# Kernel optimization log

Measured on AMD Instinct MI355X. Metric: run time of the kernel, lower is better.

Reference implementation:

```python
import jax, jax.numpy as jnp
import numpy as np

N_NODES = 50000
N_EDGES = 800000
D_IN, D_HID, D_OUT = 64, 128, 64


def _sage_conv(x, src, dst, W_l, b_l, W_r):
    # PyG SAGEConv (aggr='mean'): out = lin_l(mean_j x_j) + lin_r(x_i)
    msg = x[src]                                    # [E, d] gather
    summed = jax.ops.segment_sum(msg, dst, num_segments=N_NODES)
    cnt = jax.ops.segment_sum(jnp.ones((msg.shape[0], 1), x.dtype), dst,
                              num_segments=N_NODES)
    mean = summed / jnp.maximum(cnt, 1.0)           # [N, d]
    return mean @ W_l + b_l + x @ W_r


def setup_inputs() -> dict:
    key = jax.random.key(0)
    ks = jax.random.split(key, 8)
    x = jax.random.normal(ks[0], (N_NODES, D_IN), dtype=jnp.float32)
    edge_index = jax.random.randint(ks[1], (2, N_EDGES), 0, N_NODES, dtype=jnp.int64)
    s1 = 1.0 / np.sqrt(D_IN)
    s2 = 1.0 / np.sqrt(D_HID)
    W_l1 = jax.random.uniform(ks[2], (D_IN, D_HID), jnp.float32, -s1, s1)
    b_l1 = jnp.zeros((D_HID,), jnp.float32)
    W_r1 = jax.random.uniform(ks[3], (D_IN, D_HID), jnp.float32, -s1, s1)
    W_l2 = jax.random.uniform(ks[4], (D_HID, D_OUT), jnp.float32, -s2, s2)
    b_l2 = jnp.zeros((D_OUT,), jnp.float32)
    W_r2 = jax.random.uniform(ks[5], (D_HID, D_OUT), jnp.float32, -s2, s2)
    return {"x": x, "edge_index": edge_index,
            "W_l1": W_l1, "b_l1": b_l1, "W_r1": W_r1,
            "W_l2": W_l2, "b_l2": b_l2, "W_r2": W_r2}


def reference(x, edge_index, W_l1, b_l1, W_r1, W_l2, b_l2, W_r2):
    src, dst = edge_index[0], edge_index[1]
    h = _sage_conv(x, src, dst, W_l1, b_l1, W_r1)
    h = jax.nn.relu(h)
    # dropout is identity in eval mode (F.dropout(training=self.training))
    out = _sage_conv(h, src, dst, W_l2, b_l2, W_r2)
    return out
```

## Files before the change

kernel.cpp:

```cpp
#include <hip/hip_runtime.h>

namespace {

constexpr int NNODES = 50000;
constexpr int NEDGES = 800000;
constexpr int NBUCK  = (NNODES + 127) / 128;
constexpr int BCAP   = 3072;
constexpr int SB     = 64;
constexpr int CHUNK  = NEDGES / SB;


static __device__ __forceinline__ unsigned short f2bf(float f) {
  unsigned u = __float_as_uint(f);
  u += 0x7FFFu + ((u >> 16) & 1u);
  return (unsigned short)(u >> 16);
}

static __device__ __forceinline__ void pk_fma_lo(float2& d, const float2 a, const float2 b) {
  asm("v_pk_fma_f32 %0, %1, %2, %0 op_sel:[0,0,0] op_sel_hi:[0,1,1]"
      : "+v"(d) : "v"(a), "v"(b));
}
static __device__ __forceinline__ void pk_fma_hi(float2& d, const float2 a, const float2 b) {
  asm("v_pk_fma_f32 %0, %1, %2, %0 op_sel:[1,0,0] op_sel_hi:[1,1,1]"
      : "+v"(d) : "v"(a), "v"(b));
}

static __device__ __forceinline__ int detect_is64_block(const void* raw, int* s_tmp) {
  if (threadIdx.x == 0) *s_tmp = 0;
  __syncthreads();
  const unsigned int* w = (const unsigned int*)raw;
  const int nz = (w[1 + 2 * (int)threadIdx.x] != 0u) ? 1 : 0;
  if (nz) atomicOr(s_tmp, 1);
  __syncthreads();
  return (*s_tmp == 0) ? 1 : 0;
}

__global__ __launch_bounds__(256) void x_to_bf16(const float* __restrict__ xin,
                                                 unsigned short* __restrict__ xb) {
  const int total4 = NNODES * 64 / 4;
  const int stride = gridDim.x * blockDim.x;
  for (int t = blockIdx.x * blockDim.x + threadIdx.x; t < total4; t += stride) {
    const float4 v = ((const float4*)xin)[t];
    ushort4 o;
    o.x = f2bf(v.x); o.y = f2bf(v.y); o.z = f2bf(v.z); o.w = f2bf(v.w);
    ((ushort4*)xb)[t] = o;
  }
}

__global__ __launch_bounds__(512) void hist_pass(const void* __restrict__ raw,
                                                 int* __restrict__ blkhist) {
  __shared__ int hist[NBUCK];
  __shared__ int s_tmp;
  const int is64 = detect_is64_block(raw, &s_tmp);
  for (int i = threadIdx.x; i < NBUCK; i += 512) hist[i] = 0;
  __syncthreads();
  const int b = blockIdx.x;
  const int beg = b * CHUNK, end = beg + CHUNK;
  for (int e = beg + (int)threadIdx.x; e < end; e += 512) {
    const int d = is64 ? (int)((const long long*)raw)[NEDGES + e]
                       : ((const int*)raw)[NEDGES + e];
    atomicAdd(&hist[d >> 7], 1);
  }
  __syncthreads();
  for (int i = threadIdx.x; i < NBUCK; i += 512) blkhist[i * SB + b] = hist[i];
}

__global__ __launch_bounds__(64) void col_scan(const int* __restrict__ blkhist,
                                               int* __restrict__ offs,
                                               int* __restrict__ bcount) {
  const int bk = blockIdx.x;
  const int t = threadIdx.x;
  const int c = blkhist[bk * SB + t];
  int s = c;
#pragma unroll
  for (int off = 1; off < 64; off <<= 1) {
    const int u = __shfl_up(s, off, 64);
    if (t >= off) s += u;
  }
  offs[bk * SB + t] = bk * BCAP + (s - c);
  if (t == 63) bcount[bk] = s;
}

__global__ __launch_bounds__(512) void bucket_prefix(const int* __restrict__ bcount,
                                                     int* __restrict__ bprefix) {
  __shared__ int sh[512];
  const int t = threadIdx.x;
  const int v = (t < NBUCK) ? bcount[t] : 0;
  sh[t] = v;
  __syncthreads();
#pragma unroll
  for (int off = 1; off < 512; off <<= 1) {
    const int val = sh[t];
    const int add = (t >= off) ? sh[t - off] : 0;
    __syncthreads();
    sh[t] = val + add;
    __syncthreads();
  }
  if (t < NBUCK) bprefix[t] = sh[t] - v;
}

__global__ __launch_bounds__(512) void scatter_pass(const void* __restrict__ raw,
                                                    const int* __restrict__ offs,
                                                    unsigned int* __restrict__ ebuf) {
  __shared__ int loff[NBUCK];
  __shared__ int lcur[NBUCK];
  __shared__ int s_tmp;
  const int is64 = detect_is64_block(raw, &s_tmp);
  const int b = blockIdx.x;
  for (int i = threadIdx.x; i < NBUCK; i += 512) {
    loff[i] = offs[i * SB + b];
    lcur[i] = 0;
  }
  __syncthreads();
  const int beg = b * CHUNK, end = beg + CHUNK;
  for (int e = beg + (int)threadIdx.x; e < end; e += 512) {
    int s, d;
    if (is64) {
      const long long* p = (const long long*)raw;
      s = (int)p[e];
      d = (int)p[NEDGES + e];
    } else {
      const int* p = (const int*)raw;
      s = p[e];
      d = p[NEDGES + e];
    }
    const int bk = d >> 7;
    const unsigned int val = ((unsigned int)d << 16) | (unsigned int)s;
    const int lr = atomicAdd(&lcur[bk], 1);
    ebuf[loff[bk] + lr] = val;
  }
}

__global__ __launch_bounds__(256) void csr_emit2(const unsigned int* __restrict__ ebuf,
                                                 const int* __restrict__ bcount,
                                                 const int* __restrict__ bprefix,
                                                 int* __restrict__ row_ptr,
                                                 int* __restrict__ col) {
  const int bk = blockIdx.x;
  const int base = bk * 128;
  const int nloc = min(128, NNODES - base);
  const int cnt = bcount[bk];
  const int bbase = bprefix[bk];
  const unsigned int* eb = ebuf + (size_t)bk * BCAP;

  __shared__ int dcnt[128];
  __shared__ int loff[128];
  __shared__ int lcur[128];
  if (threadIdx.x < 128) dcnt[threadIdx.x] = 0;
  __syncthreads();

  unsigned int vals[12];
  int m = 0;
#pragma unroll
  for (int k = 0; k < 12; ++k) {
    const int e = (int)threadIdx.x + k * 256;
    if (e < cnt) {
      vals[k] = eb[e];
      atomicAdd(&dcnt[(vals[k] >> 16) & 127u], 1);
      m = k + 1;
    }
  }
  __syncthreads();

  if (threadIdx.x < 128) loff[threadIdx.x] = dcnt[threadIdx.x];
  __syncthreads();
#pragma unroll
  for (int off = 1; off < 128; off <<= 1) {
    int add = 0;
    if (threadIdx.x < 128 && (int)threadIdx.x >= off) add = loff[threadIdx.x - off];
    __syncthreads();
    if (threadIdx.x < 128) loff[threadIdx.x] += add;
    __syncthreads();
  }
  if (threadIdx.x < 128) {
    const int excl = loff[threadIdx.x] - dcnt[threadIdx.x];
    loff[threadIdx.x] = excl;
    lcur[threadIdx.x] = 0;
    if ((int)threadIdx.x < nloc) row_ptr[base + threadIdx.x] = bbase + excl;
  }
  if (bk == NBUCK - 1 && threadIdx.x == 0) row_ptr[NNODES] = NEDGES;
  __syncthreads();

#pragma unroll
  for (int k = 0; k < 12; ++k) {
    if (k < m) {
      const int loc = (int)((vals[k] >> 16) & 127u);
      const int slot = bbase + loff[loc] + atomicAdd(&lcur[loc], 1);
      col[slot] = (int)(vals[k] & 0xFFFFu);
    }
  }
}

template <bool FINAL>
__global__ __launch_bounds__(256) void seg_mean_bf(const unsigned int* __restrict__ xb2,
                                                   const int* __restrict__ row_ptr,
                                                   const int* __restrict__ col,
                                                   const float* __restrict__ radd,
                                                   float* __restrict__ outbuf) {
  const int lane = (int)(threadIdx.x & 63);
  const int half = lane >> 5;
  const int c = lane & 31;
  const int wid = (blockIdx.x * blockDim.x + threadIdx.x) >> 6;
  const int nw = (gridDim.x * blockDim.x) >> 6;
  for (int v = wid; v < NNODES; v += nw) {
    const int b = row_ptr[v];
    const int e = row_ptr[v + 1];
    float accx = 0.0f, accy = 0.0f;
    int i = b;
    for (; i + 8 <= e; i += 8) {
      const int s0 = col[i + 0 + half];
      const int s1 = col[i + 2 + half];
      const int s2 = col[i + 4 + half];
      const int s3 = col[i + 6 + half];
      const unsigned int w0 = xb2[(size_t)s0 * 32 + c];
      const unsigned int w1 = xb2[(size_t)s1 * 32 + c];
      const unsigned int w2 = xb2[(size_t)s2 * 32 + c];
      const unsigned int w3 = xb2[(size_t)s3 * 32 + c];
      accx += __uint_as_float(w0 << 16) + __uint_as_float(w1 << 16)
            + __uint_as_float(w2 << 16) + __uint_as_float(w3 << 16);
      accy += __uint_as_float(w0 & 0xFFFF0000u) + __uint_as_float(w1 & 0xFFFF0000u)
            + __uint_as_float(w2 & 0xFFFF0000u) + __uint_as_float(w3 & 0xFFFF0000u);
    }
    for (; i + 2 <= e; i += 2) {
      const unsigned int w0 = xb2[(size_t)col[i + half] * 32 + c];
      accx += __uint_as_float(w0 << 16);
      accy += __uint_as_float(w0 & 0xFFFF0000u);
    }
    if (i < e && half == 0) {
      const unsigned int w0 = xb2[(size_t)col[i] * 32 + c];
      accx += __uint_as_float(w0 << 16);
      accy += __uint_as_float(w0 & 0xFFFF0000u);
    }
    accx += __shfl_xor(accx, 32, 64);
    accy += __shfl_xor(accy, 32, 64);
    if (half == 0) {
      const float inv = 1.0f / fmaxf((float)(e - b), 1.0f);
      float2 res = make_float2(accx * inv, accy * inv);
      const size_t gi = (size_t)v * 32 + c;
      if (FINAL) {
        const float2 ra = ((const float2*)radd)[gi];
        res.x += ra.x; res.y += ra.y;
      }
      ((float2*)outbuf)[gi] = res;
    }
  }
}

template <int MODE>
__global__ __launch_bounds__(256, 3) void gemm128(const float* __restrict__ A0,
                                                  const float* __restrict__ A1,
                                                  const float* __restrict__ W0,
                                                  const float* __restrict__ W1,
                                                  const float* __restrict__ bias,
                                                  float* __restrict__ O0,
                                                  float* __restrict__ O1,
                                                  unsigned short* __restrict__ PB) {
  constexpr int SAS = 36;
  __shared__ float sA[64][SAS];
  __shared__ float sW[32][128];
  const int row0 = blockIdx.x * 64;
  const int tid = threadIdx.x;
  const int r0 = (tid >> 4) * 4;
  const int j0 = (tid & 15) * 4;

  float2 accA2[4][2];
  float2 accB2[4][2];
#pragma unroll
  for (int r = 0; r < 4; ++r)
#pragma unroll
    for (int p = 0; p < 2; ++p) {
      accA2[r][p] = make_float2(0.f, 0.f);
      accB2[r][p] = make_float2(0.f, 0.f);
    }

#pragma unroll 1
  for (int ck = 0; ck < 4; ++ck) {
#pragma unroll
    for (int v = 0; v < 2; ++v) {
      const int vid = v * 256 + tid;
      const int rr = vid >> 3;
      const int kq = (vid & 7) * 4;
      const int grow = row0 + rr;
      float4 val = make_float4(0.f, 0.f, 0.f, 0.f);
      if (grow < NNODES) {
        if (MODE == 0) {
          const float* src = (ck < 2) ? A0 : A1;
          const int kk = (ck & 1) * 32 + kq;
          val = *(const float4*)&src[(size_t)grow * 64 + kk];
        } else {
          val = *(const float4*)&A0[(size_t)grow * 128 + ck * 32 + kq];
        }
      }
      *(float4*)&sA[rr][kq] = val;
    }
#pragma unroll
    for (int v = 0; v < 4; ++v) {
      const int vid = v * 256 + tid;
      const int kk = vid >> 5;
      const int jq = (vid & 31) * 4;
      float4 w;
      if (MODE == 0) {
        const float* src = (ck < 2) ? W0 : W1;
        const int krel = (ck & 1) * 32 + kk;
        w = *(const float4*)&src[(size_t)krel * 128 + jq];
      } else {
        const int kg = ck * 32 + kk;
        const float* src = (jq < 64) ? W0 : W1;
        const int jrel = (jq < 64) ? jq : jq - 64;
        w = *(const float4*)&src[(size_t)kg * 64 + jrel];
      }
      *(float4*)&sW[kk][jq] = w;
    }
    __syncthreads();
#pragma unroll
    for (int k4 = 0; k4 < 8; ++k4) {
      float4 a[4];
#pragma unroll
      for (int r = 0; r < 4; ++r) a[r] = *(const float4*)&sA[r0 + r][k4 * 4];
#pragma unroll
      for (int kp = 0; kp < 2; ++kp) {
        const int k_even = k4 * 4 + kp * 2;
        const float4 wlo0 = *(const float4*)&sW[k_even][j0];
        const float4 whi0 = *(const float4*)&sW[k_even][64 + j0];
        const float4 wlo1 = *(const float4*)&sW[k_even + 1][j0];
        const float4 whi1 = *(const float4*)&sW[k_even + 1][64 + j0];
#pragma unroll
        for (int r = 0; r < 4; ++r) {
          const float2 ap = (kp == 0) ? make_float2(a[r].x, a[r].y)
                                      : make_float2(a[r].z, a[r].w);
          pk_fma_lo(accA2[r][0], ap, make_float2(wlo0.x, wlo0.y));
          pk_fma_lo(accA2[r][1], ap, make_float2(wlo0.z, wlo0.w));
          pk_fma_lo(accB2[r][0], ap, make_float2(whi0.x, whi0.y));
          pk_fma_lo(accB2[r][1], ap, make_float2(whi0.z, whi0.w));
          pk_fma_hi(accA2[r][0], ap, make_float2(wlo1.x, wlo1.y));
          pk_fma_hi(accA2[r][1], ap, make_float2(wlo1.z, wlo1.w));
          pk_fma_hi(accB2[r][0], ap, make_float2(whi1.x, whi1.y));
          pk_fma_hi(accB2[r][1], ap, make_float2(whi1.z, whi1.w));
        }
      }
    }
    __syncthreads();
  }

  float4 blo = make_float4(0.f, 0.f, 0.f, 0.f);
  float4 bhi;
  if (MODE == 0) {
    blo = *(const float4*)&bias[j0];
    bhi = *(const float4*)&bias[64 + j0];
  } else {
    bhi = *(const float4*)&bias[j0];
  }
#pragma unroll
  for (int r = 0; r < 4; ++r) {
    const int grow = row0 + r0 + r;
    if (grow >= NNODES) continue;
    float4 lo = make_float4(accA2[r][0].x + blo.x, accA2[r][0].y + blo.y,
                            accA2[r][1].x + blo.z, accA2[r][1].y + blo.w);
    float4 hi = make_float4(accB2[r][0].x + bhi.x, accB2[r][0].y + bhi.y,
                            accB2[r][1].x + bhi.z, accB2[r][1].y + bhi.w);
    if (MODE == 0) {
      lo.x = fmaxf(lo.x, 0.f); lo.y = fmaxf(lo.y, 0.f);
      lo.z = fmaxf(lo.z, 0.f); lo.w = fmaxf(lo.w, 0.f);
      hi.x = fmaxf(hi.x, 0.f); hi.y = fmaxf(hi.y, 0.f);
      hi.z = fmaxf(hi.z, 0.f); hi.w = fmaxf(hi.w, 0.f);
      *(float4*)&O0[(size_t)grow * 128 + j0] = lo;
      *(float4*)&O0[(size_t)grow * 128 + 64 + j0] = hi;
    } else {
      ushort4 ob;
      ob.x = f2bf(lo.x); ob.y = f2bf(lo.y); ob.z = f2bf(lo.z); ob.w = f2bf(lo.w);
      *(ushort4*)&PB[(size_t)grow * 64 + j0] = ob;
      *(float4*)&O1[(size_t)grow * 64 + j0] = hi;
    }
  }
}

}

extern "C" void kernel_launch(void* const* d_in, const int* in_sizes, int n_in,
                              void* d_out, int out_size, void* d_ws, size_t ws_size,
                              hipStream_t stream) {
  const float* x   = (const float*)d_in[0];
  const void*  ei  = d_in[1];
  const float* Wl1 = (const float*)d_in[2];
  const float* bl1 = (const float*)d_in[3];
  const float* Wr1 = (const float*)d_in[4];
  const float* Wl2 = (const float*)d_in[5];
  const float* bl2 = (const float*)d_in[6];
  const float* Wr2 = (const float*)d_in[7];
  float* out = (float*)d_out;

  char* ws = (char*)d_ws;
  int*            blkhist = (int*)(ws + 0);
  int*            offs    = (int*)(ws + 100352);
  int*            bcount  = (int*)(ws + 200704);
  int*            bprefix = (int*)(ws + 202752);
  int*            row_ptr = (int*)(ws + 204800);
  int*            col     = (int*)(ws + 404992);
  unsigned int*   ebuf    = (unsigned int*)(ws + 3604992);
  unsigned short* xb      = (unsigned short*)(ws + 8409600);
  unsigned short* pb      = (unsigned short*)(ws + 14809600);
  float*          mean1   = (float*)(ws + 21209600);
  float*          h       = (float*)(ws + 34009600);
  float*          r       = mean1;

  x_to_bf16<<<1024, 256, 0, stream>>>(x, xb);

  hist_pass<<<SB, 512, 0, stream>>>(ei, blkhist);
  col_scan<<<NBUCK, 64, 0, stream>>>(blkhist, offs, bcount);
  bucket_prefix<<<1, 512, 0, stream>>>(bcount, bprefix);
  scatter_pass<<<SB, 512, 0, stream>>>(ei, offs, ebuf);
  csr_emit2<<<NBUCK, 256, 0, stream>>>(ebuf, bcount, bprefix, row_ptr, col);

  constexpr int GEMM_BLOCKS = (NNODES + 63) / 64;

  seg_mean_bf<false><<<12500, 256, 0, stream>>>((const unsigned int*)xb, row_ptr, col,
                                                nullptr, mean1);
  gemm128<0><<<GEMM_BLOCKS, 256, 0, stream>>>(mean1, x, Wl1, Wr1, bl1, h, nullptr, nullptr);

  gemm128<1><<<GEMM_BLOCKS, 256, 0, stream>>>(h, nullptr, Wl2, Wr2, bl2, nullptr, r, pb);
  seg_mean_bf<true><<<12500, 256, 0, stream>>>((const unsigned int*)pb, row_ptr, col,
                                               r, out);
}
```

Measured before the change: 163.6 us.

## Fuse CSR build and bf16 conversion into one persistent kernel with grid barriers

Merges the bf16 conversion, histogram, column scan, scatter and per-bucket CSR emit into a single 64-block persistent kernel that uses atomic grid-wide barriers in place of separate launches. The global bucket prefix pass goes away: edges stay in padded per-bucket slots and each node gets a packed start/degree word, so the aggregation kernel reads one int instead of two row pointers. This removes several launch gaps and a scratch copy. In exchange the prep work runs on only 64 blocks, spin barriers need all blocks co-resident, and a memset is added.

```diff
diff --git a/kernel.cpp b/kernel.cpp
--- a/kernel.cpp
+++ b/kernel.cpp
@@ -25,176 +25,168 @@
       : "+v"(d) : "v"(a), "v"(b));
 }
 
+static __device__ __forceinline__ void grid_sync(int* bar, int target) {
+  __syncthreads();
+  if (threadIdx.x == 0) {
+    __threadfence();
+    atomicAdd(bar, 1);
+    while (atomicAdd(bar, 0) < target) {
+      __builtin_amdgcn_s_sleep(2);
+    }
+    __threadfence();
+  }
+  __syncthreads();
+}
+
 static __device__ __forceinline__ int detect_is64_block(const void* raw, int* s_tmp) {
   if (threadIdx.x == 0) *s_tmp = 0;
   __syncthreads();
   const unsigned int* w = (const unsigned int*)raw;
-  const int nz = (w[1 + 2 * (int)threadIdx.x] != 0u) ? 1 : 0;
+  const int nz = (w[1 + 2 * (int)(threadIdx.x & 511)] != 0u) ? 1 : 0;
   if (nz) atomicOr(s_tmp, 1);
   __syncthreads();
   return (*s_tmp == 0) ? 1 : 0;
 }
 
-__global__ __launch_bounds__(256) void x_to_bf16(const float* __restrict__ xin,
-                                                 unsigned short* __restrict__ xb) {
-  const int total4 = NNODES * 64 / 4;
-  const int stride = gridDim.x * blockDim.x;
-  for (int t = blockIdx.x * blockDim.x + threadIdx.x; t < total4; t += stride) {
+__global__ __launch_bounds__(512) void prep_mega(const void* __restrict__ raw,
+                                                 const float* __restrict__ xin,
+                                                 unsigned short* __restrict__ xb,
+                                                 int* __restrict__ blkhist,
+                                                 int* __restrict__ offs,
+                                                 int* __restrict__ bcount,
+                                                 unsigned int* __restrict__ ecol,
+                                                 int* __restrict__ rowse,
+                                                 int* __restrict__ bar) {
+  __shared__ int hist[NBUCK];
+  __shared__ int loff[NBUCK];
+  __shared__ int lcur[NBUCK];
+  __shared__ int dcnt[128];
+  __shared__ int noff[128];
+  __shared__ int ncur[128];
+  __shared__ int s_tmp;
+
+  const int b = blockIdx.x;
+  const int tid = (int)threadIdx.x;
+  const int is64 = detect_is64_block(raw, &s_tmp);
+
+  for (int t = b * 512 + tid; t < NNODES * 64 / 4; t += SB * 512) {
     const float4 v = ((const float4*)xin)[t];
     ushort4 o;
     o.x = f2bf(v.x); o.y = f2bf(v.y); o.z = f2bf(v.z); o.w = f2bf(v.w);
     ((ushort4*)xb)[t] = o;
   }
-}
-
-__global__ __launch_bounds__(512) void hist_pass(const void* __restrict__ raw,
-                                                 int* __restrict__ blkhist) {
-  __shared__ int hist[NBUCK];
-  __shared__ int s_tmp;
-  const int is64 = detect_is64_block(raw, &s_tmp);
-  for (int i = threadIdx.x; i < NBUCK; i += 512) hist[i] = 0;
-  __syncthreads();
-  const int b = blockIdx.x;
-  const int beg = b * CHUNK, end = beg + CHUNK;
-  for (int e = beg + (int)threadIdx.x; e < end; e += 512) {
-    const int d = is64 ? (int)((const long long*)raw)[NEDGES + e]
-                       : ((const int*)raw)[NEDGES + e];
-    atomicAdd(&hist[d >> 7], 1);
-  }
-  __syncthreads();
-  for (int i = threadIdx.x; i < NBUCK; i += 512) blkhist[i * SB + b] = hist[i];
-}
-
-__global__ __launch_bounds__(64) void col_scan(const int* __restrict__ blkhist,
-                                               int* __restrict__ offs,
-                                               int* __restrict__ bcount) {
-  const int bk = blockIdx.x;
-  const int t = threadIdx.x;
-  const int c = blkhist[bk * SB + t];
-  int s = c;
-#pragma unroll
-  for (int off = 1; off < 64; off <<= 1) {
-    const int u = __shfl_up(s, off, 64);
-    if (t >= off) s += u;
-  }
-  offs[bk * SB + t] = bk * BCAP + (s - c);
-  if (t == 63) bcount[bk] = s;
-}
-
-__global__ __launch_bounds__(512) void bucket_prefix(const int* __restrict__ bcount,
-                                                     int* __restrict__ bprefix) {
-  __shared__ int sh[512];
-  const int t = threadIdx.x;
-  const int v = (t < NBUCK) ? bcount[t] : 0;
-  sh[t] = v;
-  __syncthreads();
-#pragma unroll
-  for (int off = 1; off < 512; off <<= 1) {
-    const int val = sh[t];
-    const int add = (t >= off) ? sh[t - off] : 0;
-    __syncthreads();
-    sh[t] = val + add;
-    __syncthreads();
-  }
-  if (t < NBUCK) bprefix[t] = sh[t] - v;
-}
-
-__global__ __launch_bounds__(512) void scatter_pass(const void* __restrict__ raw,
-                                                    const int* __restrict__ offs,
-                                                    unsigned int* __restrict__ ebuf) {
-  __shared__ int loff[NBUCK];
-  __shared__ int lcur[NBUCK];
-  __shared__ int s_tmp;
-  const int is64 = detect_is64_block(raw, &s_tmp);
-  const int b = blockIdx.x;
-  for (int i = threadIdx.x; i < NBUCK; i += 512) {
+  for (int i = tid; i < NBUCK; i += 512) hist[i] = 0;
+  __syncthreads();
+  {
+    const int beg = b * CHUNK, end = beg + CHUNK;
+    for (int e = beg + tid; e < end; e += 512) {
+      const int d = is64 ? (int)((const long long*)raw)[NEDGES + e]
+                         : ((const int*)raw)[NEDGES + e];
+      atomicAdd(&hist[d >> 7], 1);
+    }
+  }
+  __syncthreads();
+  for (int i = tid; i < NBUCK; i += 512) blkhist[i * SB + b] = hist[i];
+
+  grid_sync(bar, SB * 1);
+
+  {
+    const int lane = tid & 63;
+    const int bk = b * 8 + (tid >> 6);
+    if (bk < NBUCK) {
+      const int c = blkhist[bk * SB + lane];
+      int s = c;
+#pragma unroll
+      for (int off = 1; off < 64; off <<= 1) {
+        const int u = __shfl_up(s, off, 64);
+        if (lane >= off) s += u;
+      }
+      offs[bk * SB + lane] = bk * BCAP + (s - c);
+      if (lane == 63) bcount[bk] = s;
+    }
+  }
+
+  grid_sync(bar, SB * 2);
+
+  for (int i = tid; i < NBUCK; i += 512) {
     loff[i] = offs[i * SB + b];
     lcur[i] = 0;
   }
   __syncthreads();
-  const int beg = b * CHUNK, end = beg + CHUNK;
-  for (int e = beg + (int)threadIdx.x; e < end; e += 512) {
-    int s, d;
-    if (is64) {
-      const long long* p = (const long long*)raw;
-      s = (int)p[e];
-      d = (int)p[NEDGES + e];
-    } else {
-      const int* p = (const int*)raw;
-      s = p[e];
-      d = p[NEDGES + e];
-    }
-    const int bk = d >> 7;
-    const unsigned int val = ((unsigned int)d << 16) | (unsigned int)s;
-    const int lr = atomicAdd(&lcur[bk], 1);
-    ebuf[loff[bk] + lr] = val;
-  }
-}
-
-__global__ __launch_bounds__(256) void csr_emit2(const unsigned int* __restrict__ ebuf,
-                                                 const int* __restrict__ bcount,
-                                                 const int* __restrict__ bprefix,
-                                                 int* __restrict__ row_ptr,
-                                                 int* __restrict__ col) {
-  const int bk = blockIdx.x;
-  const int base = bk * 128;
-  const int nloc = min(128, NNODES - base);
-  const int cnt = bcount[bk];
-  const int bbase = bprefix[bk];
-  const unsigned int* eb = ebuf + (size_t)bk * BCAP;
-
-  __shared__ int dcnt[128];
-  __shared__ int loff[128];
-  __shared__ int lcur[128];
-  if (threadIdx.x < 128) dcnt[threadIdx.x] = 0;
-  __syncthreads();
-
-  unsigned int vals[12];
-  int m = 0;
-#pragma unroll
-  for (int k = 0; k < 12; ++k) {
-    const int e = (int)threadIdx.x + k * 256;
-    if (e < cnt) {
-      vals[k] = eb[e];
-      atomicAdd(&dcnt[(vals[k] >> 16) & 127u], 1);
-      m = k + 1;
-    }
-  }
-  __syncthreads();
-
-  if (threadIdx.x < 128) loff[threadIdx.x] = dcnt[threadIdx.x];
-  __syncthreads();
-#pragma unroll
-  for (int off = 1; off < 128; off <<= 1) {
-    int add = 0;
-    if (threadIdx.x < 128 && (int)threadIdx.x >= off) add = loff[threadIdx.x - off];
-    __syncthreads();
-    if (threadIdx.x < 128) loff[threadIdx.x] += add;
-    __syncthreads();
-  }
-  if (threadIdx.x < 128) {
-    const int excl = loff[threadIdx.x] - dcnt[threadIdx.x];
-    loff[threadIdx.x] = excl;
-    lcur[threadIdx.x] = 0;
-    if ((int)threadIdx.x < nloc) row_ptr[base + threadIdx.x] = bbase + excl;
-  }
-  if (bk == NBUCK - 1 && threadIdx.x == 0) row_ptr[NNODES] = NEDGES;
-  __syncthreads();
-
-#pragma unroll
-  for (int k = 0; k < 12; ++k) {
-    if (k < m) {
-      const int loc = (int)((vals[k] >> 16) & 127u);
-      const int slot = bbase + loff[loc] + atomicAdd(&lcur[loc], 1);
-      col[slot] = (int)(vals[k] & 0xFFFFu);
-    }
+  {
+    const int beg = b * CHUNK, end = beg + CHUNK;
+    for (int e = beg + tid; e < end; e += 512) {
+      int s, d;
+      if (is64) {
+        const long long* p = (const long long*)raw;
+        s = (int)p[e];
+        d = (int)p[NEDGES + e];
+      } else {
+        const int* p = (const int*)raw;
+        s = p[e];
+        d = p[NEDGES + e];
+      }
+      const int bk = d >> 7;
+      const unsigned int val = ((unsigned int)d << 16) | (unsigned int)s;
+      const int lr = atomicAdd(&lcur[bk], 1);
+      ecol[loff[bk] + lr] = val;
+    }
+  }
+
+  grid_sync(bar, SB * 3);
+
+  for (int bk = b; bk < NBUCK; bk += SB) {
+    const int base = bk * 128;
+    const int nloc = min(128, NNODES - base);
+    const int cnt = bcount[bk];
+    unsigned int* eb = ecol + (size_t)bk * BCAP;
+    if (tid < 128) dcnt[tid] = 0;
+    __syncthreads();
+    unsigned int vals[6];
+    int m = 0;
+#pragma unroll
+    for (int k = 0; k < 6; ++k) {
+      const int e = tid + k * 512;
+      if (e < cnt) {
+        vals[k] = eb[e];
+        atomicAdd(&dcnt[(vals[k] >> 16) & 127u], 1);
+        m = k + 1;
+      }
+    }
+    __syncthreads();
+    if (tid < 128) noff[tid] = dcnt[tid];
+    __syncthreads();
+#pragma unroll
+    for (int off = 1; off < 128; off <<= 1) {
+      int add = 0;
+      if (tid < 128 && tid >= off) add = noff[tid - off];
+      __syncthreads();
+      if (tid < 128) noff[tid] += add;
+      __syncthreads();
+    }
+    if (tid < 128) {
+      const int excl = noff[tid] - dcnt[tid];
+      noff[tid] = excl;
+      ncur[tid] = 0;
+      if (tid < nloc)
+        rowse[base + tid] = ((bk * BCAP + excl) << 9) | dcnt[tid];
+    }
+    __syncthreads();
+#pragma unroll
+    for (int k = 0; k < 6; ++k) {
+      if (k < m) {
+        const int loc = (int)((vals[k] >> 16) & 127u);
+        eb[noff[loc] + atomicAdd(&ncur[loc], 1)] = vals[k] & 0xFFFFu;
+      }
+    }
+    __syncthreads();
   }
 }
 
 template <bool FINAL>
 __global__ __launch_bounds__(256) void seg_mean_bf(const unsigned int* __restrict__ xb2,
-                                                   const int* __restrict__ row_ptr,
-                                                   const int* __restrict__ col,
+                                                   const int* __restrict__ rowse,
+                                                   const unsigned int* __restrict__ col,
                                                    const float* __restrict__ radd,
                                                    float* __restrict__ outbuf) {
   const int lane = (int)(threadIdx.x & 63);
@@ -203,15 +195,16 @@
   const int wid = (blockIdx.x * blockDim.x + threadIdx.x) >> 6;
   const int nw = (gridDim.x * blockDim.x) >> 6;
   for (int v = wid; v < NNODES; v += nw) {
-    const int b = row_ptr[v];
-    const int e = row_ptr[v + 1];
+    const int se = rowse[v];
+    const int b = se >> 9;
+    const int e = b + (se & 511);
     float accx = 0.0f, accy = 0.0f;
     int i = b;
     for (; i + 8 <= e; i += 8) {
-      const int s0 = col[i + 0 + half];
-      const int s1 = col[i + 2 + half];
-      const int s2 = col[i + 4 + half];
-      const int s3 = col[i + 6 + half];
+      const int s0 = (int)col[i + 0 + half];
+      const int s1 = (int)col[i + 2 + half];
+      const int s2 = (int)col[i + 4 + half];
+      const int s3 = (int)col[i + 6 + half];
       const unsigned int w0 = xb2[(size_t)s0 * 32 + c];
       const unsigned int w1 = xb2[(size_t)s1 * 32 + c];
       const unsigned int w2 = xb2[(size_t)s2 * 32 + c];
@@ -234,7 +227,7 @@
     accx += __shfl_xor(accx, 32, 64);
     accy += __shfl_xor(accy, 32, 64);
     if (half == 0) {
-      const float inv = 1.0f / fmaxf((float)(e - b), 1.0f);
+      const float inv = 1.0f / fmaxf((float)(se & 511), 1.0f);
       float2 res = make_float2(accx * inv, accy * inv);
       const size_t gi = (size_t)v * 32 + c;
       if (FINAL) {
@@ -390,34 +383,29 @@
   float* out = (float*)d_out;
 
   char* ws = (char*)d_ws;
-  int*            blkhist = (int*)(ws + 0);
-  int*            offs    = (int*)(ws + 100352);
-  int*            bcount  = (int*)(ws + 200704);
-  int*            bprefix = (int*)(ws + 202752);
-  int*            row_ptr = (int*)(ws + 204800);
-  int*            col     = (int*)(ws + 404992);
-  unsigned int*   ebuf    = (unsigned int*)(ws + 3604992);
-  unsigned short* xb      = (unsigned short*)(ws + 8409600);
-  unsigned short* pb      = (unsigned short*)(ws + 14809600);
-  float*          mean1   = (float*)(ws + 21209600);
-  float*          h       = (float*)(ws + 34009600);
+  int*            bar     = (int*)(ws + 0);
+  int*            blkhist = (int*)(ws + 256);
+  int*            offs    = (int*)(ws + 100608);
+  int*            bcount  = (int*)(ws + 200960);
+  int*            rowse   = (int*)(ws + 203008);
+  unsigned int*   ecol    = (unsigned int*)(ws + 403200);
+  unsigned short* xb      = (unsigned short*)(ws + 5207808);
+  unsigned short* pb      = (unsigned short*)(ws + 11607808);
+  float*          mean1   = (float*)(ws + 18007808);
+  float*          h       = (float*)(ws + 30807808);
   float*          r       = mean1;
 
-  x_to_bf16<<<1024, 256, 0, stream>>>(x, xb);
-
-  hist_pass<<<SB, 512, 0, stream>>>(ei, blkhist);
-  col_scan<<<NBUCK, 64, 0, stream>>>(blkhist, offs, bcount);
-  bucket_prefix<<<1, 512, 0, stream>>>(bcount, bprefix);
-  scatter_pass<<<SB, 512, 0, stream>>>(ei, offs, ebuf);
-  csr_emit2<<<NBUCK, 256, 0, stream>>>(ebuf, bcount, bprefix, row_ptr, col);
+  hipMemsetAsync(bar, 0, 256, stream);
+
+  prep_mega<<<SB, 512, 0, stream>>>(ei, x, xb, blkhist, offs, bcount, ecol, rowse, bar);
 
   constexpr int GEMM_BLOCKS = (NNODES + 63) / 64;
 
-  seg_mean_bf<false><<<12500, 256, 0, stream>>>((const unsigned int*)xb, row_ptr, col,
+  seg_mean_bf<false><<<12500, 256, 0, stream>>>((const unsigned int*)xb, rowse, ecol,
                                                 nullptr, mean1);
   gemm128<0><<<GEMM_BLOCKS, 256, 0, stream>>>(mean1, x, Wl1, Wr1, bl1, h, nullptr, nullptr);
 
   gemm128<1><<<GEMM_BLOCKS, 256, 0, stream>>>(h, nullptr, Wl2, Wr2, bl2, nullptr, r, pb);
-  seg_mean_bf<true><<<12500, 256, 0, stream>>>((const unsigned int*)pb, row_ptr, col,
+  seg_mean_bf<true><<<12500, 256, 0, stream>>>((const unsigned int*)pb, rowse, ecol,
                                                r, out);
 }
```

Measured after the change: 192.2 us. 1.17x slower.
